# Kernel tuning notes

Hardware: AMD Instinct MI355X
Metric: run time of the kernel (lower is better)

## Reference

```python
import jax, jax.numpy as jnp
import numpy as np

NUM_VIEW, NUM_ANGLE, NUM_DEPTH = 300, 12, 4
GRASP_MAX_WIDTH = 0.1
B, N_SEED, N_GP = 2, 1024, 1024


def _views_np(n=NUM_VIEW):
    # Fibonacci-sphere view sampling (generate_grasp_views)
    phi = (np.sqrt(5.0) - 1.0) / 2.0
    i = np.arange(n, dtype=np.float64)
    z = (2.0 * i + 1.0) / n - 1.0
    r = np.sqrt(np.maximum(1.0 - z * z, 0.0))
    x = r * np.cos(2.0 * np.pi * i * phi)
    y = r * np.sin(2.0 * np.pi * i * phi)
    return np.stack([x, y, z], 1).astype(np.float32)


def _viewpoint_to_matrix(towards, angle):
    # batch_viewpoint_params_to_matrix
    ax = towards / jnp.linalg.norm(towards, axis=1, keepdims=True)
    ay = jnp.stack([-ax[:, 1], ax[:, 0], jnp.zeros_like(ax[:, 0])], 1)
    n = jnp.linalg.norm(ay, axis=1, keepdims=True)
    ay = jnp.where(n > 1e-8, ay / jnp.maximum(n, 1e-12), jnp.array([0.0, 1.0, 0.0], ax.dtype))
    az = jnp.cross(ax, ay)
    R2 = jnp.stack([ax, ay, az], axis=2)  # columns = axes
    c, s = jnp.cos(angle), jnp.sin(angle)
    o, zr = jnp.ones_like(c), jnp.zeros_like(c)
    R1 = jnp.stack([o, zr, zr, zr, c, -s, zr, s, c], 1).reshape(-1, 3, 3)
    return R2 @ R1

VIEWS = jnp.asarray(_views_np())                                   # (V,3)
_ANG = jnp.asarray((np.pi / NUM_ANGLE) * np.arange(NUM_ANGLE, dtype=np.float32))
ANGLES_REP = jnp.tile(_ANG, NUM_VIEW)
VIEWS_REP = jnp.repeat(VIEWS, NUM_ANGLE, axis=0)
GRASP_ROT = _viewpoint_to_matrix(-VIEWS_REP, ANGLES_REP)           # (V*A,3,3)
DEPTHS = jnp.linspace(0.01, 0.04, NUM_DEPTH)
SCORE_BINS = jnp.asarray([0.1, 0.2, 0.3, 0.4, 0.5, 0.6, 0.7, 0.8, 0.9], jnp.float32)
WIDTH_BINS = jnp.asarray([0.02, 0.04, 0.06, 0.08], jnp.float32)
# gripper key points in local frame for width=depth=0.02 (batch_get_key_points)
_LOCAL = jnp.asarray([[0.02, 0.0, 0.0], [0.02, 0.01, 0.0], [0.02, -0.01, 0.0], [0.0, 0.0, 0.0]], jnp.float32)
_LOCAL_SYM = _LOCAL * jnp.asarray([1.0, -1.0, 1.0], jnp.float32)


def _kp12(R, local):
    # rotate the 4 local key points, flatten to 12-dim descriptor
    return jnp.einsum('mij,kj->mki', R, local).reshape(R.shape[0], 12)


def _sqdist(a, b):
    # squared euclidean distances (M,D)x(L,D)->(M,L)
    return jnp.sum(a * a, -1)[:, None] + jnp.sum(b * b, -1)[None, :] - 2.0 * (a @ b.T)


def _rot6d_to_matrix(r6):
    a1, a2 = r6[:, :3], r6[:, 3:]
    b1 = a1 / jnp.linalg.norm(a1, axis=-1, keepdims=True)
    a2p = a2 - jnp.sum(b1 * a2, -1, keepdims=True) * b1
    b2 = a2p / jnp.linalg.norm(a2p, axis=-1, keepdims=True)
    b3 = jnp.cross(b1, b2)
    return jnp.stack([b1, b2, b3], axis=1)  # rows


def _align_angle(rot_trans, scores, widths):
    # align_angle_index: per-view angle matching with 180-deg symmetry
    V, A = NUM_VIEW, NUM_ANGLE
    pkp = _kp12(GRASP_ROT, _LOCAL).reshape(V, A, 12)
    tR = rot_trans.reshape(-1, 3, 3)
    tkp = _kp12(tR, _LOCAL).reshape(V, A, 12)
    tkps = _kp12(tR, _LOCAL_SYM).reshape(V, A, 12)
    d1 = jnp.sum((pkp[:, :, None] - tkp[:, None]) ** 2, -1)   # (V,A,A)
    d2 = jnp.sum((pkp[:, :, None] - tkps[:, None]) ** 2, -1)
    inds = jnp.where(jnp.min(d1, -1) < jnp.min(d2, -1), jnp.argmin(d1, -1), jnp.argmin(d2, -1))  # (V,A)
    rot_out = jnp.take_along_axis(rot_trans, jnp.broadcast_to(inds[:, :, None, None], rot_trans.shape), axis=1)
    idx_s = jnp.broadcast_to(inds[None, :, :, None], scores.shape)
    return rot_out, jnp.take_along_axis(scores, idx_s, 2), jnp.take_along_axis(widths, idx_s, 2)


def _match_one(seed_xyz, pose, gpoints, gscores, gwidths, rot6d, depthp):
    V, A, D = NUM_VIEW, NUM_ANGLE, NUM_DEPTH
    R, t = pose[:, :3], pose[:, 3]
    gp_trans = gpoints @ R.T + t
    views_trans = VIEWS @ R.T
    view_inds = jnp.argmin(_sqdist(VIEWS, views_trans), axis=1)             # (V,)
    rot_trans = jnp.einsum('ij,mjk->mik', R, GRASP_ROT).reshape(V, A, 3, 3)[view_inds]
    gscores = gscores[:, view_inds]
    gwidths = gwidths[:, view_inds]
    rot_trans, gscores, gwidths = _align_angle(rot_trans, gscores, gwidths)
    # nearest GT grasp point for every seed point
    nn = jnp.argmin(_sqdist(seed_xyz, gp_trans), axis=1)                    # (N,)
    gp_sel = gp_trans[nn]
    sc = gscores[nn]                                                        # (N,V,A,D)
    wd = gwidths[nn]
    # keypoint KNN of predicted rotation vs all V*A templates.
    # Pred and template key points share the same seed center and fixed
    # width/depth=0.02, so centers cancel in the distances.
    Rp = _rot6d_to_matrix(rot6d)
    pbase = _kp12(Rp, _LOCAL)                                               # (N,12)
    tR = rot_trans.reshape(-1, 3, 3)
    tbase = _kp12(tR, _LOCAL)                                               # (V*A,12)
    tbase_s = _kp12(tR, _LOCAL_SYM)
    d1 = _sqdist(pbase, tbase)
    d2 = _sqdist(pbase, tbase_s)
    rot_inds = jnp.where(jnp.min(d1, 1) < jnp.min(d2, 1), jnp.argmin(d1, 1), jnp.argmin(d2, 1))  # (N,)
    depth_inds = jnp.argmin(jnp.abs(depthp - DEPTHS[None, :]), axis=1)      # (N,)
    lin = rot_inds * D + depth_inds                                         # ravel_index
    n = seed_xyz.shape[0]
    ar = jnp.arange(n)
    gt_w = wd.reshape(n, -1)[ar, lin][:, None]
    gt_s = sc.reshape(n, -1)[ar, lin][:, None]
    gt_d = DEPTHS[depth_inds][:, None]
    gt_R = tR[rot_inds]
    gt_r6 = gt_R[:, :2, :].reshape(n, 6)                                    # matrix_to_rotation_6d
    return gp_sel, gt_r6, gt_s, gt_w, gt_d


def setup_inputs() -> dict:
    key = jax.random.key(0)
    ks = jax.random.split(key, 6)
    pc = jax.random.normal(ks[0], (B, N_SEED, 3), jnp.float32) * 0.3
    rs = np.random.RandomState(0)
    Rr = np.stack([np.linalg.qr(rs.randn(3, 3))[0] for _ in range(B)]).astype(np.float32)
    det = np.linalg.det(Rr)
    Rr[det < 0, :, 0] *= -1.0
    tt = rs.randn(B, 3, 1).astype(np.float32) * 0.1
    pose = jnp.asarray(np.concatenate([Rr, tt], axis=2))                    # (B,3,4)
    gp = jax.random.normal(ks[1], (B, N_GP, 3), jnp.float32) * 0.05
    labels = jax.random.uniform(ks[2], (B, N_GP, NUM_VIEW, NUM_ANGLE, NUM_DEPTH), jnp.float32)
    offs = jax.random.uniform(ks[3], (B, N_GP, NUM_VIEW, NUM_ANGLE, NUM_DEPTH), jnp.float32) * 0.12
    r6 = jax.random.normal(ks[4], (B, N_SEED, 6), jnp.float32)
    dpred = jax.random.uniform(ks[5], (B, N_SEED, 1), jnp.float32) * 0.05
    return {'point_clouds': pc, 'object_pose': pose, 'grasp_points': gp,
            'grasp_labels': labels, 'grasp_offsets': offs,
            'grasp_rot_pred': r6, 'grasp_depth_pred': dpred}


def reference(point_clouds, object_pose, grasp_points, grasp_labels, grasp_offsets, grasp_rot_pred, grasp_depth_pred):
    pts, rots, sc, wd, dp = jax.vmap(_match_one)(point_clouds, object_pose, grasp_points,
                                                 grasp_labels, grasp_offsets,
                                                 grasp_rot_pred, grasp_depth_pred)
    mask = (sc > 0) & (wd <= GRASP_MAX_WIDTH)
    sc = jnp.where(mask, 1.1 - sc, 0.0)
    width_ids = jnp.searchsorted(WIDTH_BINS, wd)   # torch.bucketize(right=False)
    score_ids = jnp.searchsorted(SCORE_BINS, sc)
    return pts, rots, sc, wd, dp, width_ids, score_ids
```

## Files before the change

### kernel.cpp

```cpp
#include <hip/hip_runtime.h>

#define NV 300
#define NA 12
#define ND 4
#define NM (NV*NA)
#define NS 1024
#define NG 1024

#define W_VIEWS 0
#define W_GROT  900
#define W_PKP   33300
#define W_BATCH 76500
#define SB      134032

#define PB_GPT  0
#define PB_ROT  3072
#define PB_TB   35472
#define PB_TBS  78672
#define PB_TN1  121872
#define PB_TN2  125472
#define PB_VIND 129072
#define PB_AIND 129372
#define PB_NN   132972

__constant__ float C_L[4][3]  = {{0.02f,0.f,0.f},{0.02f,0.01f,0.f},{0.02f,-0.01f,0.f},{0.f,0.f,0.f}};
__constant__ float C_LS[4][3] = {{0.02f,0.f,0.f},{0.02f,-0.01f,0.f},{0.02f,0.01f,0.f},{0.f,0.f,0.f}};

__device__ __forceinline__ void kp12(const float R[9], const float (*L)[3], float out[12]) {
#pragma unroll
    for (int k = 0; k < 4; ++k)
#pragma unroll
        for (int i = 0; i < 3; ++i)
            out[k*3+i] = R[i*3+0]*L[k][0] + R[i*3+1]*L[k][1] + R[i*3+2]*L[k][2];
}

__global__ void k_views(float* W) {
    int i = blockIdx.x*blockDim.x + threadIdx.x;
    if (i >= NV) return;
    const double PI = 3.14159265358979323846;
    double phi = (sqrt(5.0) - 1.0) * 0.5;
    double z = (2.0*i + 1.0)/(double)NV - 1.0;
    double r2 = 1.0 - z*z; r2 = r2 > 0.0 ? r2 : 0.0;
    double r = sqrt(r2);
    double ang = 2.0*PI*(double)i*phi;
    W[W_VIEWS + 3*i+0] = (float)(r*cos(ang));
    W[W_VIEWS + 3*i+1] = (float)(r*sin(ang));
    W[W_VIEWS + 3*i+2] = (float)z;
}

__global__ void k_grot(float* W) {
    int m = blockIdx.x*blockDim.x + threadIdx.x;
    if (m >= NM) return;
    int vi = m / NA, ai = m % NA;
    float tx = -W[W_VIEWS+3*vi+0], ty = -W[W_VIEWS+3*vi+1], tz = -W[W_VIEWS+3*vi+2];
    float nrm = sqrtf(tx*tx + ty*ty + tz*tz);
    float ax0 = tx/nrm, ax1 = ty/nrm, ax2 = tz/nrm;
    float ay0 = -ax1, ay1 = ax0, ay2 = 0.f;
    float n2 = sqrtf(ay0*ay0 + ay1*ay1 + ay2*ay2);
    if (n2 > 1e-8f) { float d = fmaxf(n2, 1e-12f); ay0 /= d; ay1 /= d; ay2 /= d; }
    else { ay0 = 0.f; ay1 = 1.f; ay2 = 0.f; }
    float az0 = ax1*ay2 - ax2*ay1;
    float az1 = ax2*ay0 - ax0*ay2;
    float az2 = ax0*ay1 - ax1*ay0;
    float angle = (float)(3.14159265358979323846/12.0*(double)ai);
    float c = cosf(angle), s = sinf(angle);
    float G[9];
    G[0]=ax0; G[1]=ay0*c+az0*s; G[2]=-ay0*s+az0*c;
    G[3]=ax1; G[4]=ay1*c+az1*s; G[5]=-ay1*s+az1*c;
    G[6]=ax2; G[7]=ay2*c+az2*s; G[8]=-ay2*s+az2*c;
#pragma unroll
    for (int q=0;q<9;++q) W[W_GROT + 9*m + q] = G[q];
    float pk[12]; kp12(G, C_L, pk);
#pragma unroll
    for (int q=0;q<12;++q) W[W_PKP + 12*m + q] = pk[q];
}

__global__ void k_gpt(const float* __restrict__ pose, const float* __restrict__ gp, float* W) {
    int b = blockIdx.y;
    int g = blockIdx.x*blockDim.x + threadIdx.x;
    if (g >= NG) return;
    const float* P = pose + 12*b;
    float x = gp[((size_t)b*NG+g)*3+0], y = gp[((size_t)b*NG+g)*3+1], z = gp[((size_t)b*NG+g)*3+2];
    float* o = W + W_BATCH + (size_t)b*SB + PB_GPT + 3*g;
    o[0] = P[0]*x + P[1]*y + P[2]*z  + P[3];
    o[1] = P[4]*x + P[5]*y + P[6]*z  + P[7];
    o[2] = P[8]*x + P[9]*y + P[10]*z + P[11];
}

__global__ void k_vind(const float* __restrict__ pose, float* W) {
    int b = blockIdx.y;
    const float* P = pose + 12*b;
    __shared__ float vtx[NV], vty[NV], vtz[NV], vn[NV];
    for (int i = threadIdx.x; i < NV; i += 256) {
        float x = W[W_VIEWS+3*i], y = W[W_VIEWS+3*i+1], z = W[W_VIEWS+3*i+2];
        float a = P[0]*x+P[1]*y+P[2]*z;
        float c = P[4]*x+P[5]*y+P[6]*z;
        float d = P[8]*x+P[9]*y+P[10]*z;
        vtx[i]=a; vty[i]=c; vtz[i]=d;
        vn[i] = a*a + c*c + d*d;
    }
    __syncthreads();
    int wv = threadIdx.x >> 6, lane = threadIdx.x & 63;
    int v = blockIdx.x*4 + wv;
    float x = W[W_VIEWS+3*v], y = W[W_VIEWS+3*v+1], z = W[W_VIEWS+3*v+2];
    float na = x*x + y*y + z*z;
    float best = INFINITY; int bi = 0x7fffffff;
    for (int v2 = lane; v2 < NV; v2 += 64) {
        float d = na + vn[v2] - 2.f*(x*vtx[v2] + y*vty[v2] + z*vtz[v2]);
        if (d < best) { best = d; bi = v2; }
    }
#pragma unroll
    for (int off = 32; off > 0; off >>= 1) {
        float ov = __shfl_down(best, off); int oi = __shfl_down(bi, off);
        if (ov < best || (ov == best && oi < bi)) { best = ov; bi = oi; }
    }
    if (lane == 0) ((int*)W)[W_BATCH + (size_t)b*SB + PB_VIND + v] = bi;
}

__global__ void k_align(const float* __restrict__ pose, float* W) {
    int v = blockIdx.x, b = blockIdx.y;
    float* WB = W + W_BATCH + (size_t)b*SB;
    int* IB = (int*)W + W_BATCH + (size_t)b*SB;
    int vi = IB[PB_VIND + v];
    const float* P = pose + 12*b;
    __shared__ float rtr[NA][9];
    __shared__ float tk[NA][12], tks[NA][12];
    int a = threadIdx.x;
    if (a < NA) {
        const float* G = W + W_GROT + 9*(vi*NA + a);
        float rt[9];
#pragma unroll
        for (int i=0;i<3;++i)
#pragma unroll
            for (int j=0;j<3;++j)
                rt[i*3+j] = P[i*4+0]*G[0*3+j] + P[i*4+1]*G[1*3+j] + P[i*4+2]*G[2*3+j];
#pragma unroll
        for (int q=0;q<9;++q) rtr[a][q]=rt[q];
        float t1[12], t2[12];
        kp12(rt, C_L, t1); kp12(rt, C_LS, t2);
#pragma unroll
        for (int k=0;k<12;++k) { tk[a][k]=t1[k]; tks[a][k]=t2[k]; }
    }
    __syncthreads();
    if (a < NA) {
        const float* pk = W + W_PKP + 12*(v*NA + a);
        float pkl[12];
#pragma unroll
        for (int k=0;k<12;++k) pkl[k]=pk[k];
        float m1=INFINITY, m2=INFINITY; int i1=0, i2=0;
        for (int ap=0; ap<NA; ++ap) {
            float d1=0.f, d2=0.f;
#pragma unroll
            for (int k=0;k<12;++k) {
                float e1 = pkl[k]-tk[ap][k];  d1 += e1*e1;
                float e2 = pkl[k]-tks[ap][k]; d2 += e2*e2;
            }
            if (d1 < m1) { m1=d1; i1=ap; }
            if (d2 < m2) { m2=d2; i2=ap; }
        }
        int ind = (m1 < m2) ? i1 : i2;
        int mi = v*NA + a;
        IB[PB_AIND + mi] = ind;
        float sel[9];
#pragma unroll
        for (int q=0;q<9;++q) { sel[q]=rtr[ind][q]; WB[PB_ROT + 9*mi + q] = sel[q]; }
        float tb[12], tbs[12];
        kp12(sel, C_L, tb); kp12(sel, C_LS, tbs);
        float s1=0.f, s2=0.f;
#pragma unroll
        for (int k=0;k<12;++k) {
            WB[PB_TB +k*NM+mi]=tb[k];  s1 += tb[k]*tb[k];
            WB[PB_TBS+k*NM+mi]=tbs[k]; s2 += tbs[k]*tbs[k];
        }
        WB[PB_TN1+mi]=s1; WB[PB_TN2+mi]=s2;
    }
}

__global__ void k_nn(const float* __restrict__ pc, float* W) {
    int b = blockIdx.y;
    float* WB = W + W_BATCH + (size_t)b*SB;
    __shared__ float gx[NG], gy[NG], gz[NG], gn[NG];
    for (int i = threadIdx.x; i < NG; i += 256) {
        float x = WB[PB_GPT+3*i], y = WB[PB_GPT+3*i+1], z = WB[PB_GPT+3*i+2];
        gx[i]=x; gy[i]=y; gz[i]=z; gn[i]=x*x+y*y+z*z;
    }
    __syncthreads();
    int wv = threadIdx.x >> 6, lane = threadIdx.x & 63;
    int s = blockIdx.x*4 + wv;
    float px = pc[((size_t)b*NS+s)*3+0], py = pc[((size_t)b*NS+s)*3+1], pz = pc[((size_t)b*NS+s)*3+2];
    float pn = px*px+py*py+pz*pz;
    float best = INFINITY; int bi = 0x7fffffff;
    for (int g = lane; g < NG; g += 64) {
        float d = pn + gn[g] - 2.f*(px*gx[g]+py*gy[g]+pz*gz[g]);
        if (d < best) { best = d; bi = g; }
    }
#pragma unroll
    for (int off = 32; off > 0; off >>= 1) {
        float ov = __shfl_down(best, off); int oi = __shfl_down(bi, off);
        if (ov < best || (ov == best && oi < bi)) { best = ov; bi = oi; }
    }
    if (lane == 0) ((int*)W)[W_BATCH + (size_t)b*SB + PB_NN + s] = bi;
}

__global__ void k_final(const float* __restrict__ r6p, const float* __restrict__ dpp,
                        const float* __restrict__ labels, const float* __restrict__ offsets,
                        float* __restrict__ W, float* __restrict__ out, int B) {
    int b = blockIdx.y;
    int s = blockIdx.x;
    int tid = threadIdx.x;
    int wv = tid >> 6, lane = tid & 63;
    float* WB = W + W_BATCH + (size_t)b*SB;
    const int* IB = (const int*)W + W_BATCH + (size_t)b*SB;

    const float* r6 = r6p + 6*((size_t)b*NS+s);
    float a1x=r6[0],a1y=r6[1],a1z=r6[2],a2x=r6[3],a2y=r6[4],a2z=r6[5];
    float n1 = sqrtf(a1x*a1x+a1y*a1y+a1z*a1z);
    float b1x=a1x/n1, b1y=a1y/n1, b1z=a1z/n1;
    float dt = b1x*a2x+b1y*a2y+b1z*a2z;
    float p2x=a2x-dt*b1x, p2y=a2y-dt*b1y, p2z=a2z-dt*b1z;
    float n2 = sqrtf(p2x*p2x+p2y*p2y+p2z*p2z);
    float b2x=p2x/n2, b2y=p2y/n2, b2z=p2z/n2;
    float b3x=b1y*b2z-b1z*b2y, b3y=b1z*b2x-b1x*b2z, b3z=b1x*b2y-b1y*b2x;
    float Rp[9] = {b1x,b1y,b1z, b2x,b2y,b2z, b3x,b3y,b3z};
    float pb[12]; kp12(Rp, C_L, pb);
    float Pn = 0.f;
#pragma unroll
    for (int k=0;k<12;++k) Pn += pb[k]*pb[k];

    float m1=INFINITY, m2=INFINITY; int i1=0x7fffffff, i2=0x7fffffff;
#pragma unroll
    for (int it = 0; it < 4; ++it) {
        int j0 = it*1024 + tid*4;
        if (j0 < NM) {
            float dot1[4] = {0.f,0.f,0.f,0.f};
            float dot2[4] = {0.f,0.f,0.f,0.f};
#pragma unroll
            for (int k=0;k<12;++k) {
                float4 tb  = *reinterpret_cast<const float4*>(&WB[PB_TB  + k*NM + j0]);
                float4 tbs = *reinterpret_cast<const float4*>(&WB[PB_TBS + k*NM + j0]);
                dot1[0] += pb[k]*tb.x;  dot1[1] += pb[k]*tb.y;
                dot1[2] += pb[k]*tb.z;  dot1[3] += pb[k]*tb.w;
                dot2[0] += pb[k]*tbs.x; dot2[1] += pb[k]*tbs.y;
                dot2[2] += pb[k]*tbs.z; dot2[3] += pb[k]*tbs.w;
            }
            float4 tn1 = *reinterpret_cast<const float4*>(&WB[PB_TN1 + j0]);
            float4 tn2 = *reinterpret_cast<const float4*>(&WB[PB_TN2 + j0]);
            float n1v[4] = {tn1.x,tn1.y,tn1.z,tn1.w};
            float n2v[4] = {tn2.x,tn2.y,tn2.z,tn2.w};
#pragma unroll
            for (int q=0;q<4;++q) {
                float d1 = Pn + n1v[q] - 2.f*dot1[q];
                float d2 = Pn + n2v[q] - 2.f*dot2[q];
                int j = j0 + q;
                if (d1 < m1) { m1=d1; i1=j; }
                if (d2 < m2) { m2=d2; i2=j; }
            }
        }
    }
#pragma unroll
    for (int off = 32; off > 0; off >>= 1) {
        float o1 = __shfl_down(m1, off); int oi1 = __shfl_down(i1, off);
        if (o1 < m1 || (o1 == m1 && oi1 < i1)) { m1 = o1; i1 = oi1; }
        float o2 = __shfl_down(m2, off); int oi2 = __shfl_down(i2, off);
        if (o2 < m2 || (o2 == m2 && oi2 < i2)) { m2 = o2; i2 = oi2; }
    }
    __shared__ float sm1[4], sm2[4];
    __shared__ int   si1[4], si2[4];
    if (lane == 0) { sm1[wv]=m1; si1[wv]=i1; sm2[wv]=m2; si2[wv]=i2; }
    __syncthreads();
    if (tid != 0) return;
#pragma unroll
    for (int w = 1; w < 4; ++w) {
        if (sm1[w] < m1 || (sm1[w] == m1 && si1[w] < i1)) { m1 = sm1[w]; i1 = si1[w]; }
        if (sm2[w] < m2 || (sm2[w] == m2 && si2[w] < i2)) { m2 = sm2[w]; i2 = si2[w]; }
    }
    int rot_ind = (m1 < m2) ? i1 : i2;

    float dp = dpp[(size_t)b*NS+s];
    float bd = INFINITY; int di = 0;
#pragma unroll
    for (int d = 0; d < ND; ++d) {
        float dv = (float)(0.01 + 0.01*(double)d);
        float ad = fabsf(dp - dv);
        if (ad < bd) { bd = ad; di = d; }
    }

    int nn_s = IB[PB_NN+s];
    int v_out = rot_ind / NA;
    int vi = IB[PB_VIND + v_out];
    int ai = IB[PB_AIND + rot_ind];
    size_t lidx = ((((size_t)b*NG+nn_s)*NV + vi)*NA + ai)*ND + di;
    float gs = labels[lidx];
    float gw = offsets[lidx];

    int bs = b*NS + s;
    int oRot = B*NS*3;
    int oSc  = oRot + B*NS*6;
    int oWd  = oSc  + B*NS;
    int oDp  = oWd  + B*NS;
    int oWid = oDp  + B*NS;
    int oSid = oWid + B*NS;

    const float* gsel = WB + PB_GPT + 3*nn_s;
    out[3*bs+0]=gsel[0]; out[3*bs+1]=gsel[1]; out[3*bs+2]=gsel[2];
    const float* Rsel = WB + PB_ROT + 9*rot_ind;
#pragma unroll
    for (int q=0;q<6;++q) out[oRot + 6*bs + q] = Rsel[q];

    bool mask = (gs > 0.f) && (gw <= 0.1f);
    float sc = mask ? (1.1f - gs) : 0.f;
    out[oSc + bs] = sc;
    out[oWd + bs] = gw;
    out[oDp + bs] = (float)(0.01 + 0.01*(double)di);

    int wid = 0;
    wid += (0.02f < gw); wid += (0.04f < gw); wid += (0.06f < gw); wid += (0.08f < gw);
    const float sbins[9] = {0.1f,0.2f,0.3f,0.4f,0.5f,0.6f,0.7f,0.8f,0.9f};
    int sid = 0;
#pragma unroll
    for (int i=0;i<9;++i) sid += (sbins[i] < sc) ? 1 : 0;
    out[oWid + bs] = (float)wid;
    out[oSid + bs] = (float)sid;
}

extern "C" void kernel_launch(void* const* d_in, const int* in_sizes, int n_in,
                              void* d_out, int out_size, void* d_ws, size_t ws_size,
                              hipStream_t stream) {
    const float* pc      = (const float*)d_in[0];
    const float* pose    = (const float*)d_in[1];
    const float* gp      = (const float*)d_in[2];
    const float* labels  = (const float*)d_in[3];
    const float* offsets = (const float*)d_in[4];
    const float* r6      = (const float*)d_in[5];
    const float* dpp     = (const float*)d_in[6];
    float* W   = (float*)d_ws;
    float* out = (float*)d_out;
    int B = in_sizes[1] / 12;

    hipLaunchKernelGGL(k_views, dim3(2), dim3(256), 0, stream, W);
    hipLaunchKernelGGL(k_grot,  dim3((NM+255)/256), dim3(256), 0, stream, W);
    hipLaunchKernelGGL(k_gpt,   dim3(NG/256, B), dim3(256), 0, stream, pose, gp, W);
    hipLaunchKernelGGL(k_vind,  dim3(NV/4, B), dim3(256), 0, stream, pose, W);
    hipLaunchKernelGGL(k_align, dim3(NV, B), dim3(64), 0, stream, pose, W);
    hipLaunchKernelGGL(k_nn,    dim3(NS/4, B), dim3(256), 0, stream, pc, W);
    hipLaunchKernelGGL(k_final, dim3(NS, B), dim3(256), 0, stream, r6, dpp, labels, offsets, W, out, B);
}
```

Baseline: 266.3 us.

## Fuse seven setup and matching kernels into three launches

Merges view generation, grasp rotation and grasp-point transform into one setup kernel, with views recomputed inline instead of read back. View-index search is folded into the align kernel, and the point-cloud nearest-neighbour search is folded into the final matching kernel. This cuts launch count and the inter-kernel dependency gaps. In exchange, every final block now reloads all 1024 grasp points into shared memory, and the per-thread double-precision view computation is repeated.

```diff
diff --git a/kernel.cpp b/kernel.cpp
--- a/kernel.cpp
+++ b/kernel.cpp
@@ -34,64 +34,76 @@
             out[k*3+i] = R[i*3+0]*L[k][0] + R[i*3+1]*L[k][1] + R[i*3+2]*L[k][2];
 }
 
-__global__ void k_views(float* W) {
-    int i = blockIdx.x*blockDim.x + threadIdx.x;
-    if (i >= NV) return;
+__device__ __forceinline__ void view_d(int i, float* vx, float* vy, float* vz) {
     const double PI = 3.14159265358979323846;
     double phi = (sqrt(5.0) - 1.0) * 0.5;
     double z = (2.0*i + 1.0)/(double)NV - 1.0;
     double r2 = 1.0 - z*z; r2 = r2 > 0.0 ? r2 : 0.0;
     double r = sqrt(r2);
     double ang = 2.0*PI*(double)i*phi;
-    W[W_VIEWS + 3*i+0] = (float)(r*cos(ang));
-    W[W_VIEWS + 3*i+1] = (float)(r*sin(ang));
-    W[W_VIEWS + 3*i+2] = (float)z;
-}
-
-__global__ void k_grot(float* W) {
-    int m = blockIdx.x*blockDim.x + threadIdx.x;
-    if (m >= NM) return;
-    int vi = m / NA, ai = m % NA;
-    float tx = -W[W_VIEWS+3*vi+0], ty = -W[W_VIEWS+3*vi+1], tz = -W[W_VIEWS+3*vi+2];
-    float nrm = sqrtf(tx*tx + ty*ty + tz*tz);
-    float ax0 = tx/nrm, ax1 = ty/nrm, ax2 = tz/nrm;
-    float ay0 = -ax1, ay1 = ax0, ay2 = 0.f;
-    float n2 = sqrtf(ay0*ay0 + ay1*ay1 + ay2*ay2);
-    if (n2 > 1e-8f) { float d = fmaxf(n2, 1e-12f); ay0 /= d; ay1 /= d; ay2 /= d; }
-    else { ay0 = 0.f; ay1 = 1.f; ay2 = 0.f; }
-    float az0 = ax1*ay2 - ax2*ay1;
-    float az1 = ax2*ay0 - ax0*ay2;
-    float az2 = ax0*ay1 - ax1*ay0;
-    float angle = (float)(3.14159265358979323846/12.0*(double)ai);
-    float c = cosf(angle), s = sinf(angle);
-    float G[9];
-    G[0]=ax0; G[1]=ay0*c+az0*s; G[2]=-ay0*s+az0*c;
-    G[3]=ax1; G[4]=ay1*c+az1*s; G[5]=-ay1*s+az1*c;
-    G[6]=ax2; G[7]=ay2*c+az2*s; G[8]=-ay2*s+az2*c;
-#pragma unroll
-    for (int q=0;q<9;++q) W[W_GROT + 9*m + q] = G[q];
-    float pk[12]; kp12(G, C_L, pk);
-#pragma unroll
-    for (int q=0;q<12;++q) W[W_PKP + 12*m + q] = pk[q];
-}
-
-__global__ void k_gpt(const float* __restrict__ pose, const float* __restrict__ gp, float* W) {
-    int b = blockIdx.y;
-    int g = blockIdx.x*blockDim.x + threadIdx.x;
-    if (g >= NG) return;
+    *vx = (float)(r*cos(ang));
+    *vy = (float)(r*sin(ang));
+    *vz = (float)z;
+}
+
+__global__ void k_setup(const float* __restrict__ pose, const float* __restrict__ gp,
+                        float* W) {
+    int bid = blockIdx.x;
+    if (bid < 15) {
+        int m = bid*256 + threadIdx.x;
+        if (m >= NM) return;
+        if (m < NV) {
+            float x,y,z; view_d(m, &x,&y,&z);
+            W[W_VIEWS + 3*m+0] = x; W[W_VIEWS + 3*m+1] = y; W[W_VIEWS + 3*m+2] = z;
+        }
+        int vi = m / NA, ai = m % NA;
+        float vx,vy,vz; view_d(vi, &vx,&vy,&vz);
+        float tx = -vx, ty = -vy, tz = -vz;
+        float nrm = sqrtf(tx*tx + ty*ty + tz*tz);
+        float ax0 = tx/nrm, ax1 = ty/nrm, ax2 = tz/nrm;
+        float ay0 = -ax1, ay1 = ax0, ay2 = 0.f;
+        float n2 = sqrtf(ay0*ay0 + ay1*ay1 + ay2*ay2);
+        if (n2 > 1e-8f) { float d = fmaxf(n2, 1e-12f); ay0 /= d; ay1 /= d; ay2 /= d; }
+        else { ay0 = 0.f; ay1 = 1.f; ay2 = 0.f; }
+        float az0 = ax1*ay2 - ax2*ay1;
+        float az1 = ax2*ay0 - ax0*ay2;
+        float az2 = ax0*ay1 - ax1*ay0;
+        float angle = (float)(3.14159265358979323846/12.0*(double)ai);
+        float c = cosf(angle), s = sinf(angle);
+        float G[9];
+        G[0]=ax0; G[1]=ay0*c+az0*s; G[2]=-ay0*s+az0*c;
+        G[3]=ax1; G[4]=ay1*c+az1*s; G[5]=-ay1*s+az1*c;
+        G[6]=ax2; G[7]=ay2*c+az2*s; G[8]=-ay2*s+az2*c;
+#pragma unroll
+        for (int q=0;q<9;++q) W[W_GROT + 9*m + q] = G[q];
+        float pk[12]; kp12(G, C_L, pk);
+#pragma unroll
+        for (int q=0;q<12;++q) W[W_PKP + 12*m + q] = pk[q];
+    } else {
+        int idx = (bid-15)*256 + threadIdx.x;
+        int b = idx >> 10, g = idx & (NG-1);
+        const float* P = pose + 12*b;
+        float x = gp[(size_t)idx*3+0], y = gp[(size_t)idx*3+1], z = gp[(size_t)idx*3+2];
+        float* o = W + W_BATCH + (size_t)b*SB + PB_GPT + 3*g;
+        o[0] = P[0]*x + P[1]*y + P[2]*z  + P[3];
+        o[1] = P[4]*x + P[5]*y + P[6]*z  + P[7];
+        o[2] = P[8]*x + P[9]*y + P[10]*z + P[11];
+    }
+}
+
+__global__ void k_va(const float* __restrict__ pose, float* W) {
+    int v = blockIdx.x, b = blockIdx.y;
+    float* WB = W + W_BATCH + (size_t)b*SB;
+    int* IB = (int*)W + W_BATCH + (size_t)b*SB;
     const float* P = pose + 12*b;
-    float x = gp[((size_t)b*NG+g)*3+0], y = gp[((size_t)b*NG+g)*3+1], z = gp[((size_t)b*NG+g)*3+2];
-    float* o = W + W_BATCH + (size_t)b*SB + PB_GPT + 3*g;
-    o[0] = P[0]*x + P[1]*y + P[2]*z  + P[3];
-    o[1] = P[4]*x + P[5]*y + P[6]*z  + P[7];
-    o[2] = P[8]*x + P[9]*y + P[10]*z + P[11];
-}
-
-__global__ void k_vind(const float* __restrict__ pose, float* W) {
-    int b = blockIdx.y;
-    const float* P = pose + 12*b;
+    int lane = threadIdx.x;
+
     __shared__ float vtx[NV], vty[NV], vtz[NV], vn[NV];
-    for (int i = threadIdx.x; i < NV; i += 256) {
+    __shared__ float rtr[NA][9];
+    __shared__ float tk[NA][12], tks[NA][12];
+    __shared__ int s_vi;
+
+    for (int i = lane; i < NV; i += 64) {
         float x = W[W_VIEWS+3*i], y = W[W_VIEWS+3*i+1], z = W[W_VIEWS+3*i+2];
         float a = P[0]*x+P[1]*y+P[2]*z;
         float c = P[4]*x+P[5]*y+P[6]*z;
@@ -100,32 +112,24 @@
         vn[i] = a*a + c*c + d*d;
     }
     __syncthreads();
-    int wv = threadIdx.x >> 6, lane = threadIdx.x & 63;
-    int v = blockIdx.x*4 + wv;
-    float x = W[W_VIEWS+3*v], y = W[W_VIEWS+3*v+1], z = W[W_VIEWS+3*v+2];
-    float na = x*x + y*y + z*z;
-    float best = INFINITY; int bi = 0x7fffffff;
-    for (int v2 = lane; v2 < NV; v2 += 64) {
-        float d = na + vn[v2] - 2.f*(x*vtx[v2] + y*vty[v2] + z*vtz[v2]);
-        if (d < best) { best = d; bi = v2; }
-    }
-#pragma unroll
-    for (int off = 32; off > 0; off >>= 1) {
-        float ov = __shfl_down(best, off); int oi = __shfl_down(bi, off);
-        if (ov < best || (ov == best && oi < bi)) { best = ov; bi = oi; }
-    }
-    if (lane == 0) ((int*)W)[W_BATCH + (size_t)b*SB + PB_VIND + v] = bi;
-}
-
-__global__ void k_align(const float* __restrict__ pose, float* W) {
-    int v = blockIdx.x, b = blockIdx.y;
-    float* WB = W + W_BATCH + (size_t)b*SB;
-    int* IB = (int*)W + W_BATCH + (size_t)b*SB;
-    int vi = IB[PB_VIND + v];
-    const float* P = pose + 12*b;
-    __shared__ float rtr[NA][9];
-    __shared__ float tk[NA][12], tks[NA][12];
-    int a = threadIdx.x;
+    {
+        float x = W[W_VIEWS+3*v], y = W[W_VIEWS+3*v+1], z = W[W_VIEWS+3*v+2];
+        float na = x*x + y*y + z*z;
+        float best = INFINITY; int bi = 0x7fffffff;
+        for (int v2 = lane; v2 < NV; v2 += 64) {
+            float d = na + vn[v2] - 2.f*(x*vtx[v2] + y*vty[v2] + z*vtz[v2]);
+            if (d < best) { best = d; bi = v2; }
+        }
+#pragma unroll
+        for (int off = 32; off > 0; off >>= 1) {
+            float ov = __shfl_down(best, off); int oi = __shfl_down(bi, off);
+            if (ov < best || (ov == best && oi < bi)) { best = ov; bi = oi; }
+        }
+        if (lane == 0) { s_vi = bi; IB[PB_VIND + v] = bi; }
+    }
+    __syncthreads();
+    int vi = s_vi;
+    int a = lane;
     if (a < NA) {
         const float* G = W + W_GROT + 9*(vi*NA + a);
         float rt[9];
@@ -176,41 +180,38 @@
     }
 }
 
-__global__ void k_nn(const float* __restrict__ pc, float* W) {
-    int b = blockIdx.y;
-    float* WB = W + W_BATCH + (size_t)b*SB;
-    __shared__ float gx[NG], gy[NG], gz[NG], gn[NG];
-    for (int i = threadIdx.x; i < NG; i += 256) {
-        float x = WB[PB_GPT+3*i], y = WB[PB_GPT+3*i+1], z = WB[PB_GPT+3*i+2];
-        gx[i]=x; gy[i]=y; gz[i]=z; gn[i]=x*x+y*y+z*z;
-    }
-    __syncthreads();
-    int wv = threadIdx.x >> 6, lane = threadIdx.x & 63;
-    int s = blockIdx.x*4 + wv;
-    float px = pc[((size_t)b*NS+s)*3+0], py = pc[((size_t)b*NS+s)*3+1], pz = pc[((size_t)b*NS+s)*3+2];
-    float pn = px*px+py*py+pz*pz;
-    float best = INFINITY; int bi = 0x7fffffff;
-    for (int g = lane; g < NG; g += 64) {
-        float d = pn + gn[g] - 2.f*(px*gx[g]+py*gy[g]+pz*gz[g]);
-        if (d < best) { best = d; bi = g; }
-    }
-#pragma unroll
-    for (int off = 32; off > 0; off >>= 1) {
-        float ov = __shfl_down(best, off); int oi = __shfl_down(bi, off);
-        if (ov < best || (ov == best && oi < bi)) { best = ov; bi = oi; }
-    }
-    if (lane == 0) ((int*)W)[W_BATCH + (size_t)b*SB + PB_NN + s] = bi;
-}
-
-__global__ void k_final(const float* __restrict__ r6p, const float* __restrict__ dpp,
-                        const float* __restrict__ labels, const float* __restrict__ offsets,
-                        float* __restrict__ W, float* __restrict__ out, int B) {
+__global__ void k_nf(const float* __restrict__ pc,
+                     const float* __restrict__ r6p, const float* __restrict__ dpp,
+                     const float* __restrict__ labels, const float* __restrict__ offsets,
+                     float* __restrict__ W, float* __restrict__ out, int B) {
     int b = blockIdx.y;
     int s = blockIdx.x;
     int tid = threadIdx.x;
     int wv = tid >> 6, lane = tid & 63;
     float* WB = W + W_BATCH + (size_t)b*SB;
     const int* IB = (const int*)W + W_BATCH + (size_t)b*SB;
+
+    __shared__ float gx[NG], gy[NG], gz[NG], gn[NG];
+    for (int i = tid; i < NG; i += 256) {
+        float x = WB[PB_GPT+3*i], y = WB[PB_GPT+3*i+1], z = WB[PB_GPT+3*i+2];
+        gx[i]=x; gy[i]=y; gz[i]=z; gn[i]=x*x+y*y+z*z;
+    }
+    __syncthreads();
+
+    float px = pc[((size_t)b*NS+s)*3+0], py = pc[((size_t)b*NS+s)*3+1], pz = pc[((size_t)b*NS+s)*3+2];
+    float pn = px*px+py*py+pz*pz;
+    float nbest = INFINITY; int nbi = 0x7fffffff;
+    for (int g = tid; g < NG; g += 256) {
+        float d = pn + gn[g] - 2.f*(px*gx[g]+py*gy[g]+pz*gz[g]);
+        if (d < nbest) { nbest = d; nbi = g; }
+    }
+#pragma unroll
+    for (int off = 32; off > 0; off >>= 1) {
+        float ov = __shfl_down(nbest, off); int oi = __shfl_down(nbi, off);
+        if (ov < nbest || (ov == nbest && oi < nbi)) { nbest = ov; nbi = oi; }
+    }
+    __shared__ float snv[4]; __shared__ int sni[4];
+    if (lane == 0) { snv[wv] = nbest; sni[wv] = nbi; }
 
     const float* r6 = r6p + 6*((size_t)b*NS+s);
     float a1x=r6[0],a1y=r6[1],a1z=r6[2],a2x=r6[3],a2y=r6[4],a2z=r6[5];
@@ -273,8 +274,10 @@
     for (int w = 1; w < 4; ++w) {
         if (sm1[w] < m1 || (sm1[w] == m1 && si1[w] < i1)) { m1 = sm1[w]; i1 = si1[w]; }
         if (sm2[w] < m2 || (sm2[w] == m2 && si2[w] < i2)) { m2 = sm2[w]; i2 = si2[w]; }
+        if (snv[w] < nbest || (snv[w] == nbest && sni[w] < nbi)) { nbest = snv[w]; nbi = sni[w]; }
     }
     int rot_ind = (m1 < m2) ? i1 : i2;
+    int nn_s = nbi;
 
     float dp = dpp[(size_t)b*NS+s];
     float bd = INFINITY; int di = 0;
@@ -285,7 +288,6 @@
         if (ad < bd) { bd = ad; di = d; }
     }
 
-    int nn_s = IB[PB_NN+s];
     int v_out = rot_ind / NA;
     int vi = IB[PB_VIND + v_out];
     int ai = IB[PB_AIND + rot_ind];
@@ -301,8 +303,7 @@
     int oWid = oDp  + B*NS;
     int oSid = oWid + B*NS;
 
-    const float* gsel = WB + PB_GPT + 3*nn_s;
-    out[3*bs+0]=gsel[0]; out[3*bs+1]=gsel[1]; out[3*bs+2]=gsel[2];
+    out[3*bs+0]=gx[nn_s]; out[3*bs+1]=gy[nn_s]; out[3*bs+2]=gz[nn_s];
     const float* Rsel = WB + PB_ROT + 9*rot_ind;
 #pragma unroll
     for (int q=0;q<6;++q) out[oRot + 6*bs + q] = Rsel[q];
@@ -337,11 +338,8 @@
     float* out = (float*)d_out;
     int B = in_sizes[1] / 12;
 
-    hipLaunchKernelGGL(k_views, dim3(2), dim3(256), 0, stream, W);
-    hipLaunchKernelGGL(k_grot,  dim3((NM+255)/256), dim3(256), 0, stream, W);
-    hipLaunchKernelGGL(k_gpt,   dim3(NG/256, B), dim3(256), 0, stream, pose, gp, W);
-    hipLaunchKernelGGL(k_vind,  dim3(NV/4, B), dim3(256), 0, stream, pose, W);
-    hipLaunchKernelGGL(k_align, dim3(NV, B), dim3(64), 0, stream, pose, W);
-    hipLaunchKernelGGL(k_nn,    dim3(NS/4, B), dim3(256), 0, stream, pc, W);
-    hipLaunchKernelGGL(k_final, dim3(NS, B), dim3(256), 0, stream, r6, dpp, labels, offsets, W, out, B);
-}
+    hipLaunchKernelGGL(k_setup, dim3(15 + B*(NG/256)), dim3(256), 0, stream, pose, gp, W);
+    hipLaunchKernelGGL(k_va,    dim3(NV, B), dim3(64), 0, stream, pose, W);
+    hipLaunchKernelGGL(k_nf,    dim3(NS, B), dim3(256), 0, stream,
+                       pc, r6, dpp, labels, offsets, W, out, B);
+}
```

Result: faster. 260.7 us (-2.1%).
